# Performance work log

Measured on AMD Instinct MI355X. Metric: run time of the kernel, lower is better.

The kernel has to match this reference:

```python
import jax, jax.numpy as jnp
import numpy as np

B, C, H, W = 8, 512, 32, 32
NUM_HEADS = 8
NUM_GROUPS = 32
EPS = 1e-5


def setup_inputs() -> dict:
    key = jax.random.key(0)
    k1, k2, k3 = jax.random.split(key, 3)
    x = jax.random.normal(k1, (B, C, H, W), dtype=jnp.float32)
    gn_w = jnp.ones((C,), dtype=jnp.float32)
    gn_b = jnp.zeros((C,), dtype=jnp.float32)
    qkv_w = jax.random.normal(k2, (3 * C, C), dtype=jnp.float32) * 0.02
    qkv_b = jnp.zeros((3 * C,), dtype=jnp.float32)
    # NOTE: original zero-initializes proj_out; we use random weights so the
    # residual branch is non-trivial for correctness testing.
    proj_w = jax.random.normal(k3, (C, C), dtype=jnp.float32) * 0.02
    proj_b = jnp.zeros((C,), dtype=jnp.float32)
    return {"x": x, "gn_w": gn_w, "gn_b": gn_b, "qkv_w": qkv_w,
            "qkv_b": qkv_b, "proj_w": proj_w, "proj_b": proj_b}


def _group_norm(x, w, b):
    # x: [B, C, T]
    Bn, Cn, T = x.shape
    xg = x.reshape(Bn, NUM_GROUPS, Cn // NUM_GROUPS, T)
    mean = xg.mean(axis=(2, 3), keepdims=True)
    var = xg.var(axis=(2, 3), keepdims=True)
    xn = ((xg - mean) * jax.lax.rsqrt(var + EPS)).reshape(Bn, Cn, T)
    return xn * w[None, :, None] + b[None, :, None]


def reference(x, gn_w, gn_b, qkv_w, qkv_b, proj_w, proj_b):
    b, c = x.shape[0], x.shape[1]
    spatial = x.shape[2:]
    xr = x.reshape(b, c, -1)                      # [B, C, T]
    xn = _group_norm(xr, gn_w, gn_b)
    # 1x1 conv1d: [3C, C] x [B, C, T] -> [B, 3C, T]
    qkv = jnp.einsum('oc,bct->bot', qkv_w, xn) + qkv_b[None, :, None]
    T = qkv.shape[-1]
    qkv = qkv.reshape(b * NUM_HEADS, -1, T)       # [B*Nh, 3*ch, T]
    ch = qkv.shape[1] // 3
    q, k, v = jnp.split(qkv, 3, axis=1)
    scale = 1.0 / np.sqrt(np.sqrt(ch))
    weight = jnp.einsum('bct,bcs->bts', q * scale, k * scale)  # [B*Nh, T, T]
    weight = jax.nn.softmax(weight.astype(jnp.float32), axis=-1).astype(weight.dtype)
    h = jnp.einsum('bts,bcs->bct', weight, v)     # [B*Nh, ch, T]
    h = h.reshape(b, c, T)
    h = jnp.einsum('oc,bct->bot', proj_w, h) + proj_b[None, :, None]
    return (xr + h).reshape(b, c, *spatial)
```

## Files before the change

### kernel.cpp

```cpp
#include <hip/hip_runtime.h>
#include <math.h>

#define Bn 8
#define Cn 512
#define Tn 1024

typedef __attribute__((ext_vector_type(8))) short bf16x8;
typedef __attribute__((ext_vector_type(4))) float f32x4;

__device__ __forceinline__ unsigned short f2bf(float f) {
  unsigned int u = __builtin_bit_cast(unsigned int, f);
  u = (u + 0x7FFFu + ((u >> 16) & 1u)) >> 16;
  return (unsigned short)u;
}

__device__ __forceinline__ unsigned int cvtpk_bf16(float lo, float hi) {
  unsigned int r;
  asm("v_cvt_pk_bf16_f32 %0, %1, %2" : "=v"(r) : "v"(lo), "v"(hi));
  return r;
}

typedef __attribute__((address_space(1))) const unsigned int GU32;
typedef __attribute__((address_space(3))) unsigned int LU32;
__device__ __forceinline__ void gld16(const unsigned short* g, unsigned short* l) {
  __builtin_amdgcn_global_load_lds((GU32*)g, (LU32*)l, 16, 0, 0);
}

__device__ __forceinline__ void stage128x64(const unsigned short* __restrict__ src,
                                            size_t row_stride, unsigned short* lds, int tid) {
  const int w = tid >> 6;
  const int row = tid >> 3;
  const int sc = (tid & 7) ^ ((tid >> 3) & 7);
#pragma unroll
  for (int c = 0; c < 4; ++c)
    gld16(src + (size_t)(c * 32 + row) * row_stride + sc * 8,
          (unsigned short*)((char*)lds + c * 4096 + w * 1024));
}

__device__ __forceinline__ void stage64x64(const unsigned short* __restrict__ src,
                                           size_t row_stride, unsigned short* lds, int tid) {
  const int w = tid >> 6;
  const int row = tid >> 3;
  const int sc = (tid & 7) ^ ((tid >> 3) & 7);
#pragma unroll
  for (int c = 0; c < 2; ++c)
    gld16(src + (size_t)(c * 32 + row) * row_stride + sc * 8,
          (unsigned short*)((char*)lds + c * 4096 + w * 1024));
}

__global__ __launch_bounds__(256) void gn_kernel(const float* __restrict__ x,
                                                 const float* __restrict__ gw,
                                                 const float* __restrict__ gb,
                                                 unsigned short* __restrict__ xn_t) {
  const int blk = blockIdx.x;
  const int b = blk >> 5, g = blk & 31;
  const size_t base = ((size_t)b * Cn + (size_t)g * 16) * Tn;
  const float4* __restrict__ xin = (const float4*)(x + base);
  const int tid = threadIdx.x;

  float vv[16][4];
  float sum = 0.f, sq = 0.f;
#pragma unroll
  for (int k = 0; k < 16; ++k) {
    const float4 t4 = xin[tid + (k << 8)];
    vv[k][0] = t4.x; vv[k][1] = t4.y; vv[k][2] = t4.z; vv[k][3] = t4.w;
    sum += t4.x + t4.y + t4.z + t4.w;
    sq += t4.x * t4.x + t4.y * t4.y + t4.z * t4.z + t4.w * t4.w;
  }

  __shared__ float rs[8];
  const int lane = tid & 63, wv = tid >> 6;
#pragma unroll
  for (int off = 32; off > 0; off >>= 1) {
    sum += __shfl_down(sum, off);
    sq += __shfl_down(sq, off);
  }
  if (lane == 0) { rs[wv] = sum; rs[4 + wv] = sq; }
  __syncthreads();
  const float ts = rs[0] + rs[1] + rs[2] + rs[3];
  const float tq = rs[4] + rs[5] + rs[6] + rs[7];
  const float mean = ts * (1.f / 16384.f);
  const float var = tq * (1.f / 16384.f) - mean * mean;
  const float rstd = rsqrtf(var + 1e-5f);

  float aa[16], bb[16];
#pragma unroll
  for (int k = 0; k < 16; ++k) {
    aa[k] = rstd * gw[g * 16 + k];
    bb[k] = gb[g * 16 + k] - mean * aa[k];
  }

#pragma unroll
  for (int j = 0; j < 4; ++j) {
    const int t = tid * 4 + j;
    unsigned int pk[8];
#pragma unroll
    for (int k2 = 0; k2 < 8; ++k2) {
      const unsigned int lo = f2bf(vv[2 * k2][j] * aa[2 * k2] + bb[2 * k2]);
      const unsigned int hi = f2bf(vv[2 * k2 + 1][j] * aa[2 * k2 + 1] + bb[2 * k2 + 1]);
      pk[k2] = lo | (hi << 16);
    }
    unsigned short* dst = xn_t + ((size_t)(b * Tn + t)) * Cn + g * 16;
    *(uint4*)dst = make_uint4(pk[0], pk[1], pk[2], pk[3]);
    *((uint4*)dst + 1) = make_uint4(pk[4], pk[5], pk[6], pk[7]);
  }
}

__global__ __launch_bounds__(256) void cvt_kernel(const float* __restrict__ src,
                                                  unsigned short* __restrict__ dst, int n4) {
  const int i = blockIdx.x * 256 + threadIdx.x;
  if (i < n4) {
    const float4 f = ((const float4*)src)[i];
    uint2 o;
    o.x = (unsigned int)f2bf(f.x) | ((unsigned int)f2bf(f.y) << 16);
    o.y = (unsigned int)f2bf(f.z) | ((unsigned int)f2bf(f.w) << 16);
    ((uint2*)dst)[i] = o;
  }
}

__global__ __launch_bounds__(256, 2) void qkv_gemm(const unsigned short* __restrict__ Wb,
                                                   const unsigned short* __restrict__ Xb,
                                                   const float* __restrict__ bias,
                                                   unsigned short* __restrict__ q_t,
                                                   unsigned short* __restrict__ k_t,
                                                   unsigned short* __restrict__ v_t) {
  __shared__ unsigned short As[2][8192];
  __shared__ unsigned short Bs[2][8192];
  const int id = blockIdx.x;
  const int b = id & 7;
  const int inner = id >> 3;
  const int bx = inner % 12, by = inner / 12;
  const int o0 = bx * 128, t0 = by * 128;
  const int tid = threadIdx.x, lane = tid & 63, w = tid >> 6;
  const int wr = w >> 1, wc = w & 1;
  const int ln = lane & 15, g16 = lane >> 4;
  const unsigned short* __restrict__ X = Xb + (size_t)b * Tn * Cn;
  const unsigned short* __restrict__ Wt = Wb + (size_t)o0 * 512;
  const unsigned short* __restrict__ Xt = X + (size_t)t0 * 512;

  f32x4 acc[4][4];
#pragma unroll
  for (int mt = 0; mt < 4; ++mt)
#pragma unroll
    for (int nt = 0; nt < 4; ++nt) acc[mt][nt] = (f32x4){0.f, 0.f, 0.f, 0.f};

  stage128x64(Wt, 512, &As[0][0], tid);
  stage128x64(Xt, 512, &Bs[0][0], tid);
  __syncthreads();

  int buf = 0;
  for (int k0 = 0; k0 < 512; k0 += 64) {
    if (k0 + 64 < 512) {
      stage128x64(Wt + k0 + 64, 512, &As[buf ^ 1][0], tid);
      stage128x64(Xt + k0 + 64, 512, &Bs[buf ^ 1][0], tid);
    }
    const char* Ab = (const char*)&As[buf][0];
    const char* Bb = (const char*)&Bs[buf][0];
    bf16x8 af[4][2], bfr[4][2];
#pragma unroll
    for (int mt = 0; mt < 4; ++mt)
#pragma unroll
      for (int kk = 0; kk < 2; ++kk) {
        const int row = wr * 64 + mt * 16 + ln;
        const int c16 = ((kk << 2) | g16) ^ (ln & 7);
        af[mt][kk] = *(const bf16x8*)(Ab + row * 128 + (c16 << 4));
      }
#pragma unroll
    for (int nt = 0; nt < 4; ++nt)
#pragma unroll
      for (int kk = 0; kk < 2; ++kk) {
        const int row = wc * 64 + nt * 16 + ln;
        const int c16 = ((kk << 2) | g16) ^ (ln & 7);
        bfr[nt][kk] = *(const bf16x8*)(Bb + row * 128 + (c16 << 4));
      }
#pragma unroll
    for (int kk = 0; kk < 2; ++kk)
#pragma unroll
      for (int mt = 0; mt < 4; ++mt)
#pragma unroll
        for (int nt = 0; nt < 4; ++nt)
          acc[mt][nt] =
              __builtin_amdgcn_mfma_f32_16x16x32_bf16(af[mt][kk], bfr[nt][kk], acc[mt][nt], 0, 0, 0);
    __syncthreads();
    buf ^= 1;
  }

  const int o_base = o0 + wr * 64, t_base = t0 + wc * 64;
  const int partw = (o_base >> 6) % 3;
  const int bh = b * 8 + o_base / 192;
  unsigned short (*Vlds)[136] = (unsigned short (*)[136])(&As[0][0]);

  if (partw < 2) {
    unsigned short* qk = (partw == 0 ? q_t : k_t) + (size_t)bh * 65536;
    const float sc = (partw == 0) ? 0.18033688f : 1.0f;
#pragma unroll
    for (int mt = 0; mt < 4; ++mt) {
      const int ob16 = o_base + mt * 16;
      float bv[4];
#pragma unroll
      for (int r = 0; r < 4; ++r) bv[r] = bias[ob16 + g16 * 4 + r];
#pragma unroll
      for (int nt = 0; nt < 4; ++nt) {
        const int t = t_base + nt * 16 + ln;
        const float v0 = (acc[mt][nt][0] + bv[0]) * sc;
        const float v1 = (acc[mt][nt][1] + bv[1]) * sc;
        const float v2 = (acc[mt][nt][2] + bv[2]) * sc;
        const float v3 = (acc[mt][nt][3] + bv[3]) * sc;
        uint2 pk;
        pk.x = (unsigned int)f2bf(v0) | ((unsigned int)f2bf(v1) << 16);
        pk.y = (unsigned int)f2bf(v2) | ((unsigned int)f2bf(v3) << 16);
        *(uint2*)(qk + (size_t)t * 64 + mt * 16 + g16 * 4) = pk;
      }
    }
  } else {
#pragma unroll
    for (int mt = 0; mt < 4; ++mt) {
      float bv[4];
#pragma unroll
      for (int r = 0; r < 4; ++r) bv[r] = bias[o_base + mt * 16 + g16 * 4 + r];
#pragma unroll
      for (int nt = 0; nt < 4; ++nt)
#pragma unroll
        for (int r = 0; r < 4; ++r)
          Vlds[mt * 16 + g16 * 4 + r][wc * 64 + nt * 16 + ln] = f2bf(acc[mt][nt][r] + bv[r]);
    }
  }
  __syncthreads();
  const int bxm = bx % 3;
  if (bxm) {
    const int o_first = o0 + (bxm - 1) * 64;
    unsigned short* vdst = v_t + (size_t)(b * 8 + o_first / 192) * 65536;
    const int c = tid >> 2, tseg = (tid & 3) << 5;
    const unsigned short* src = &Vlds[c][tseg];
    unsigned short* p = vdst + (size_t)c * Tn + t0 + tseg;
    const uint4 d0 = *(const uint4*)(src);
    const uint4 d1 = *(const uint4*)(src + 8);
    const uint4 d2 = *(const uint4*)(src + 16);
    const uint4 d3 = *(const uint4*)(src + 24);
    *(uint4*)(p) = d0;
    *(uint4*)(p + 8) = d1;
    *(uint4*)(p + 16) = d2;
    *(uint4*)(p + 24) = d3;
  }
}

__global__ __launch_bounds__(256, 3) void attn_kernel(const unsigned short* __restrict__ q_t,
                                                      const unsigned short* __restrict__ k_t,
                                                      const unsigned short* __restrict__ v_t,
                                                      unsigned short* __restrict__ h_t) {
  __shared__ unsigned short Ks[2][4096];
  __shared__ unsigned short Vs[2][4096];
  __shared__ __align__(16) unsigned short P_lds[4][1024];
  const int id = blockIdx.x;
  const int xcd = id & 7, qq = id >> 3;
  const int bh = ((qq >> 4) << 3) | xcd;
  const int tc = qq & 15;
  const int tid = threadIdx.x, lane = tid & 63, w = tid >> 6;
  const int t_wave = tc * 64 + w * 16;
  const int ln = lane & 15, g16 = lane >> 4, g8 = g16 * 8;
  const unsigned short* __restrict__ qbase = q_t + (size_t)bh * 65536;
  const unsigned short* __restrict__ kbase = k_t + (size_t)bh * 65536;
  const unsigned short* __restrict__ vbase = v_t + (size_t)bh * 65536;
  char* __restrict__ Pb = (char*)P_lds[w];

  int koff[4][2];
#pragma unroll
  for (int f = 0; f < 4; ++f)
#pragma unroll
    for (int kb = 0; kb < 2; ++kb)
      koff[f][kb] = (f * 16 + ln) * 128 + ((((kb << 2) | g16) ^ (ln & 7)) << 4);

  int wr_off[4], rd_off[2];
#pragma unroll
  for (int ns = 0; ns < 4; ++ns)
    wr_off[ns] = ln * 128 + ((((ns << 1) | (g16 >> 1)) ^ (ln & 7)) << 4) + ((g16 & 1) << 3);
#pragma unroll
  for (int kb = 0; kb < 2; ++kb)
    rd_off[kb] = ln * 128 + ((((kb << 2) | g16) ^ (ln & 7)) << 4);

  bf16x8 qf[2];
#pragma unroll
  for (int kb = 0; kb < 2; ++kb)
    qf[kb] = *(const bf16x8*)(qbase + (size_t)(t_wave + ln) * 64 + kb * 32 + g8);

  f32x4 o_acc[4];
#pragma unroll
  for (int nc = 0; nc < 4; ++nc) o_acc[nc] = (f32x4){0.f, 0.f, 0.f, 0.f};
  float m_run = -1e30f, l_run = 0.f;

  stage64x64(kbase, 64, &Ks[0][0], tid);
  stage64x64(vbase, 1024, &Vs[0][0], tid);
  __syncthreads();

  int buf = 0;
  for (int st = 0; st < 16; ++st) {
    const int s0 = st << 6;
    if (st < 15) {
      stage64x64(kbase + (size_t)(s0 + 64) * 64, 64, &Ks[buf ^ 1][0], tid);
      stage64x64(vbase + (s0 + 64), 1024, &Vs[buf ^ 1][0], tid);
    }
    const char* Kb = (const char*)&Ks[buf][0];
    const char* Vb = (const char*)&Vs[buf][0];

    bf16x8 kf[4][2];
#pragma unroll
    for (int ns = 0; ns < 4; ++ns)
#pragma unroll
      for (int kb = 0; kb < 2; ++kb)
        kf[ns][kb] = *(const bf16x8*)(Kb + koff[ns][kb]);

    f32x4 sacc[4];
#pragma unroll
    for (int ns = 0; ns < 4; ++ns) sacc[ns] = (f32x4){0.f, 0.f, 0.f, 0.f};

    __builtin_amdgcn_s_setprio(1);
#pragma unroll
    for (int kb = 0; kb < 2; ++kb)
#pragma unroll
      for (int ns = 0; ns < 4; ++ns)
        sacc[ns] = __builtin_amdgcn_mfma_f32_16x16x32_bf16(kf[ns][kb], qf[kb], sacc[ns], 0, 0, 0);
    __builtin_amdgcn_s_setprio(0);

    bf16x8 vf[4][2];
#pragma unroll
    for (int nc = 0; nc < 4; ++nc)
#pragma unroll
      for (int kb = 0; kb < 2; ++kb)
        vf[nc][kb] = *(const bf16x8*)(Vb + koff[nc][kb]);

    float m = sacc[0][0];
#pragma unroll
    for (int ns = 0; ns < 4; ++ns)
#pragma unroll
      for (int r = 0; r < 4; ++r) m = fmaxf(m, sacc[ns][r]);
    m = fmaxf(m, __shfl_xor(m, 16));
    m = fmaxf(m, __shfl_xor(m, 32));

    if (__any((m > m_run + 11.f) ? 1 : 0)) {
      const float mnew = fmaxf(m_run, m);
      const float al = __builtin_amdgcn_exp2f(m_run - mnew);
      m_run = mnew;
      l_run *= al;
      float al4[4];
#pragma unroll
      for (int r = 0; r < 4; ++r) al4[r] = __shfl(al, (g16 << 2) + r);
#pragma unroll
      for (int nc = 0; nc < 4; ++nc)
#pragma unroll
        for (int r = 0; r < 4; ++r) o_acc[nc][r] *= al4[r];
    }

    float rsum = 0.f;
#pragma unroll
    for (int ns = 0; ns < 4; ++ns) {
#pragma unroll
      for (int r = 0; r < 4; ++r) {
        sacc[ns][r] = __builtin_amdgcn_exp2f(sacc[ns][r] - m_run);
        rsum += sacc[ns][r];
      }
    }
    rsum += __shfl_xor(rsum, 16);
    rsum += __shfl_xor(rsum, 32);
    l_run += rsum;

#pragma unroll
    for (int ns = 0; ns < 4; ++ns) {
      uint2 pk2;
      pk2.x = cvtpk_bf16(sacc[ns][0], sacc[ns][1]);
      pk2.y = cvtpk_bf16(sacc[ns][2], sacc[ns][3]);
      *(uint2*)(Pb + wr_off[ns]) = pk2;
    }
    bf16x8 pf[2];
#pragma unroll
    for (int kb = 0; kb < 2; ++kb) pf[kb] = *(const bf16x8*)(Pb + rd_off[kb]);

    __builtin_amdgcn_s_setprio(1);
#pragma unroll
    for (int kb = 0; kb < 2; ++kb)
#pragma unroll
      for (int nc = 0; nc < 4; ++nc)
        o_acc[nc] = __builtin_amdgcn_mfma_f32_16x16x32_bf16(pf[kb], vf[nc][kb], o_acc[nc], 0, 0, 0);
    __builtin_amdgcn_s_setprio(0);

    __syncthreads();
    buf ^= 1;
  }

  const float rl = 1.f / l_run;
  float rl4[4];
#pragma unroll
  for (int r = 0; r < 4; ++r) rl4[r] = __shfl(rl, (g16 << 2) + r);
  const int b = bh >> 3, hh = bh & 7;
  unsigned short* __restrict__ hb = h_t + (size_t)b * Tn * Cn + hh * 64;
#pragma unroll
  for (int nc = 0; nc < 4; ++nc) {
    const int c = nc * 16 + ln;
#pragma unroll
    for (int r = 0; r < 4; ++r) {
      const int t = t_wave + g16 * 4 + r;
      hb[(size_t)t * Cn + c] = f2bf(o_acc[nc][r] * rl4[r]);
    }
  }
}

__global__ __launch_bounds__(256, 2) void proj_gemm(const unsigned short* __restrict__ Wb,
                                                    const unsigned short* __restrict__ Hb,
                                                    const float* __restrict__ pbias,
                                                    const float* __restrict__ x,
                                                    float* __restrict__ out) {
  __shared__ unsigned short As[2][8192];
  __shared__ unsigned short Bs[2][8192];
  const int id = blockIdx.x;
  const int b = id & 7;
  const int inner = id >> 3;
  const int bx = inner & 3, by = inner >> 2;
  const int o0 = bx * 128, t0 = by * 128;
  const int tid = threadIdx.x, lane = tid & 63, w = tid >> 6;
  const int wr = w >> 1, wc = w & 1;
  const int ln = lane & 15, g16 = lane >> 4;
  const unsigned short* __restrict__ H = Hb + (size_t)b * Tn * Cn;
  const unsigned short* __restrict__ Wt = Wb + (size_t)o0 * 512;
  const unsigned short* __restrict__ Ht = H + (size_t)t0 * 512;

  f32x4 acc[4][4];
#pragma unroll
  for (int mt = 0; mt < 4; ++mt)
#pragma unroll
    for (int nt = 0; nt < 4; ++nt) acc[mt][nt] = (f32x4){0.f, 0.f, 0.f, 0.f};

  stage128x64(Wt, 512, &As[0][0], tid);
  stage128x64(Ht, 512, &Bs[0][0], tid);
  __syncthreads();

  int buf = 0;
  for (int k0 = 0; k0 < 512; k0 += 64) {
    if (k0 + 64 < 512) {
      stage128x64(Wt + k0 + 64, 512, &As[buf ^ 1][0], tid);
      stage128x64(Ht + k0 + 64, 512, &Bs[buf ^ 1][0], tid);
    }
    const char* Ab = (const char*)&As[buf][0];
    const char* Bb = (const char*)&Bs[buf][0];
    bf16x8 af[4][2], bfr[4][2];
#pragma unroll
    for (int mt = 0; mt < 4; ++mt)
#pragma unroll
      for (int kk = 0; kk < 2; ++kk) {
        const int row = wr * 64 + mt * 16 + ln;
        const int c16 = ((kk << 2) | g16) ^ (ln & 7);
        af[mt][kk] = *(const bf16x8*)(Ab + row * 128 + (c16 << 4));
      }
#pragma unroll
    for (int nt = 0; nt < 4; ++nt)
#pragma unroll
      for (int kk = 0; kk < 2; ++kk) {
        const int row = wc * 64 + nt * 16 + ln;
        const int c16 = ((kk << 2) | g16) ^ (ln & 7);
        bfr[nt][kk] = *(const bf16x8*)(Bb + row * 128 + (c16 << 4));
      }
#pragma unroll
    for (int kk = 0; kk < 2; ++kk)
#pragma unroll
      for (int mt = 0; mt < 4; ++mt)
#pragma unroll
        for (int nt = 0; nt < 4; ++nt)
          acc[mt][nt] =
              __builtin_amdgcn_mfma_f32_16x16x32_bf16(af[mt][kk], bfr[nt][kk], acc[mt][nt], 0, 0, 0);
    __syncthreads();
    buf ^= 1;
  }

  const int o_base = o0 + wr * 64, t_base = t0 + wc * 64;
#pragma unroll
  for (int mt = 0; mt < 4; ++mt) {
    const int ob = o_base + mt * 16 + g16 * 4;
    float pb[4];
#pragma unroll
    for (int r = 0; r < 4; ++r) pb[r] = pbias[ob + r];
#pragma unroll
    for (int nt = 0; nt < 4; ++nt) {
      const int t = t_base + nt * 16 + ln;
#pragma unroll
      for (int r = 0; r < 4; ++r) {
        const size_t idx = (size_t)b * Cn * Tn + (size_t)(ob + r) * Tn + t;
        out[idx] = acc[mt][nt][r] + pb[r] + x[idx];
      }
    }
  }
}

extern "C" void kernel_launch(void* const* d_in, const int* in_sizes, int n_in,
                              void* d_out, int out_size, void* d_ws, size_t ws_size,
                              hipStream_t stream) {
  (void)in_sizes; (void)n_in; (void)out_size; (void)ws_size;
  const float* x = (const float*)d_in[0];
  const float* gn_w = (const float*)d_in[1];
  const float* gn_b = (const float*)d_in[2];
  const float* qkv_w = (const float*)d_in[3];
  const float* qkv_b = (const float*)d_in[4];
  const float* proj_w = (const float*)d_in[5];
  const float* proj_b = (const float*)d_in[6];
  float* out = (float*)d_out;

  unsigned short* wsu = (unsigned short*)d_ws;
  unsigned short* xn_t = wsu;
  unsigned short* wqkv = xn_t + (size_t)4194304;
  unsigned short* wproj = wqkv + (size_t)786432;
  unsigned short* q_t = wproj + (size_t)262144;
  unsigned short* k_t = q_t + (size_t)4194304;
  unsigned short* v_t = k_t + (size_t)4194304;
  unsigned short* h_t = v_t + (size_t)4194304;

  gn_kernel<<<dim3(256), 256, 0, stream>>>(x, gn_w, gn_b, xn_t);
  cvt_kernel<<<dim3(768), 256, 0, stream>>>(qkv_w, wqkv, 196608);
  cvt_kernel<<<dim3(256), 256, 0, stream>>>(proj_w, wproj, 65536);
  qkv_gemm<<<dim3(768), 256, 0, stream>>>(wqkv, xn_t, qkv_b, q_t, k_t, v_t);
  attn_kernel<<<dim3(1024), 256, 0, stream>>>(q_t, k_t, v_t, h_t);
  proj_gemm<<<dim3(256), 256, 0, stream>>>(wproj, h_t, proj_b, x, out);
}
```

Before: 158.0 us.

## Process two query tiles per wave in attention and merge weight conversions

Each attention wave now handles 32 query rows (two 16-row M tiles) instead of 16. Every K/V fragment read from LDS therefore feeds twice as many MFMAs, and the block count is halved. This raises register use: launch bounds drop from 3 to 2 blocks per CU, and the P staging buffer doubles. The two fp32-to-bf16 weight conversion launches are also merged into one kernel to save a launch.

```diff
diff --git a/kernel.cpp b/kernel.cpp
--- a/kernel.cpp
+++ b/kernel.cpp
@@ -106,16 +106,19 @@
   }
 }
 
-__global__ __launch_bounds__(256) void cvt_kernel(const float* __restrict__ src,
-                                                  unsigned short* __restrict__ dst, int n4) {
-  const int i = blockIdx.x * 256 + threadIdx.x;
-  if (i < n4) {
-    const float4 f = ((const float4*)src)[i];
-    uint2 o;
-    o.x = (unsigned int)f2bf(f.x) | ((unsigned int)f2bf(f.y) << 16);
-    o.y = (unsigned int)f2bf(f.z) | ((unsigned int)f2bf(f.w) << 16);
-    ((uint2*)dst)[i] = o;
-  }
+__global__ __launch_bounds__(256) void cvt2_kernel(const float* __restrict__ qkv_w,
+                                                   const float* __restrict__ proj_w,
+                                                   unsigned short* __restrict__ wqkv,
+                                                   unsigned short* __restrict__ wproj) {
+  const int blk = blockIdx.x;
+  const float* src = (blk < 768) ? qkv_w : proj_w;
+  unsigned short* dst = (blk < 768) ? wqkv : wproj;
+  const int i = ((blk < 768) ? blk : blk - 768) * 256 + threadIdx.x;
+  const float4 f = ((const float4*)src)[i];
+  uint2 o;
+  o.x = (unsigned int)f2bf(f.x) | ((unsigned int)f2bf(f.y) << 16);
+  o.y = (unsigned int)f2bf(f.z) | ((unsigned int)f2bf(f.w) << 16);
+  ((uint2*)dst)[i] = o;
 }
 
 __global__ __launch_bounds__(256, 2) void qkv_gemm(const unsigned short* __restrict__ Wb,
@@ -244,19 +247,19 @@
   }
 }
 
-__global__ __launch_bounds__(256, 3) void attn_kernel(const unsigned short* __restrict__ q_t,
+__global__ __launch_bounds__(256, 2) void attn_kernel(const unsigned short* __restrict__ q_t,
                                                       const unsigned short* __restrict__ k_t,
                                                       const unsigned short* __restrict__ v_t,
                                                       unsigned short* __restrict__ h_t) {
   __shared__ unsigned short Ks[2][4096];
   __shared__ unsigned short Vs[2][4096];
-  __shared__ __align__(16) unsigned short P_lds[4][1024];
+  __shared__ __align__(16) unsigned short P_lds[4][2048];
   const int id = blockIdx.x;
   const int xcd = id & 7, qq = id >> 3;
-  const int bh = ((qq >> 4) << 3) | xcd;
-  const int tc = qq & 15;
+  const int b = qq >> 3, tc = qq & 7;
+  const int bh = b * 8 + xcd;
   const int tid = threadIdx.x, lane = tid & 63, w = tid >> 6;
-  const int t_wave = tc * 64 + w * 16;
+  const int t_wave = tc * 128 + w * 32;
   const int ln = lane & 15, g16 = lane >> 4, g8 = g16 * 8;
   const unsigned short* __restrict__ qbase = q_t + (size_t)bh * 65536;
   const unsigned short* __restrict__ kbase = k_t + (size_t)bh * 65536;
@@ -278,15 +281,19 @@
   for (int kb = 0; kb < 2; ++kb)
     rd_off[kb] = ln * 128 + ((((kb << 2) | g16) ^ (ln & 7)) << 4);
 
-  bf16x8 qf[2];
-#pragma unroll
-  for (int kb = 0; kb < 2; ++kb)
-    qf[kb] = *(const bf16x8*)(qbase + (size_t)(t_wave + ln) * 64 + kb * 32 + g8);
-
-  f32x4 o_acc[4];
-#pragma unroll
-  for (int nc = 0; nc < 4; ++nc) o_acc[nc] = (f32x4){0.f, 0.f, 0.f, 0.f};
-  float m_run = -1e30f, l_run = 0.f;
+  bf16x8 qf[2][2];
+#pragma unroll
+  for (int mt = 0; mt < 2; ++mt)
+#pragma unroll
+    for (int kb = 0; kb < 2; ++kb)
+      qf[mt][kb] = *(const bf16x8*)(qbase + (size_t)(t_wave + mt * 16 + ln) * 64 + kb * 32 + g8);
+
+  f32x4 o_acc[2][4];
+#pragma unroll
+  for (int mt = 0; mt < 2; ++mt)
+#pragma unroll
+    for (int nc = 0; nc < 4; ++nc) o_acc[mt][nc] = (f32x4){0.f, 0.f, 0.f, 0.f};
+  float m_run[2] = {-1e30f, -1e30f}, l_run[2] = {0.f, 0.f};
 
   stage64x64(kbase, 64, &Ks[0][0], tid);
   stage64x64(vbase, 1024, &Vs[0][0], tid);
@@ -309,17 +316,82 @@
       for (int kb = 0; kb < 2; ++kb)
         kf[ns][kb] = *(const bf16x8*)(Kb + koff[ns][kb]);
 
-    f32x4 sacc[4];
-#pragma unroll
-    for (int ns = 0; ns < 4; ++ns) sacc[ns] = (f32x4){0.f, 0.f, 0.f, 0.f};
+    f32x4 sacc[2][4];
+#pragma unroll
+    for (int mt = 0; mt < 2; ++mt)
+#pragma unroll
+      for (int ns = 0; ns < 4; ++ns) sacc[mt][ns] = (f32x4){0.f, 0.f, 0.f, 0.f};
 
     __builtin_amdgcn_s_setprio(1);
 #pragma unroll
     for (int kb = 0; kb < 2; ++kb)
 #pragma unroll
+      for (int ns = 0; ns < 4; ++ns) {
+        sacc[0][ns] = __builtin_amdgcn_mfma_f32_16x16x32_bf16(kf[ns][kb], qf[0][kb], sacc[0][ns], 0, 0, 0);
+        sacc[1][ns] = __builtin_amdgcn_mfma_f32_16x16x32_bf16(kf[ns][kb], qf[1][kb], sacc[1][ns], 0, 0, 0);
+      }
+    __builtin_amdgcn_s_setprio(0);
+
+    float m[2];
+#pragma unroll
+    for (int mt = 0; mt < 2; ++mt) {
+      float mm = sacc[mt][0][0];
+#pragma unroll
       for (int ns = 0; ns < 4; ++ns)
-        sacc[ns] = __builtin_amdgcn_mfma_f32_16x16x32_bf16(kf[ns][kb], qf[kb], sacc[ns], 0, 0, 0);
-    __builtin_amdgcn_s_setprio(0);
+#pragma unroll
+        for (int r = 0; r < 4; ++r) mm = fmaxf(mm, sacc[mt][ns][r]);
+      mm = fmaxf(mm, __shfl_xor(mm, 16));
+      mm = fmaxf(mm, __shfl_xor(mm, 32));
+      m[mt] = mm;
+    }
+
+    const bool need = (m[0] > m_run[0] + 11.f) || (m[1] > m_run[1] + 11.f);
+    if (__any(need ? 1 : 0)) {
+#pragma unroll
+      for (int mt = 0; mt < 2; ++mt) {
+        const float mnew = fmaxf(m_run[mt], m[mt]);
+        const float al = __builtin_amdgcn_exp2f(m_run[mt] - mnew);
+        m_run[mt] = mnew;
+        l_run[mt] *= al;
+        float al4[4];
+#pragma unroll
+        for (int r = 0; r < 4; ++r) al4[r] = __shfl(al, (g16 << 2) + r);
+#pragma unroll
+        for (int nc = 0; nc < 4; ++nc)
+#pragma unroll
+          for (int r = 0; r < 4; ++r) o_acc[mt][nc][r] *= al4[r];
+      }
+    }
+
+#pragma unroll
+    for (int mt = 0; mt < 2; ++mt) {
+      float rsum = 0.f;
+#pragma unroll
+      for (int ns = 0; ns < 4; ++ns) {
+#pragma unroll
+        for (int r = 0; r < 4; ++r) {
+          sacc[mt][ns][r] = __builtin_amdgcn_exp2f(sacc[mt][ns][r] - m_run[mt]);
+          rsum += sacc[mt][ns][r];
+        }
+      }
+      rsum += __shfl_xor(rsum, 16);
+      rsum += __shfl_xor(rsum, 32);
+      l_run[mt] += rsum;
+#pragma unroll
+      for (int ns = 0; ns < 4; ++ns) {
+        uint2 pk2;
+        pk2.x = cvtpk_bf16(sacc[mt][ns][0], sacc[mt][ns][1]);
+        pk2.y = cvtpk_bf16(sacc[mt][ns][2], sacc[mt][ns][3]);
+        *(uint2*)(Pb + mt * 2048 + wr_off[ns]) = pk2;
+      }
+    }
+
+    bf16x8 pf[2][2];
+#pragma unroll
+    for (int mt = 0; mt < 2; ++mt)
+#pragma unroll
+      for (int kb = 0; kb < 2; ++kb)
+        pf[mt][kb] = *(const bf16x8*)(Pb + mt * 2048 + rd_off[kb]);
 
     bf16x8 vf[4][2];
 #pragma unroll
@@ -328,77 +400,36 @@
       for (int kb = 0; kb < 2; ++kb)
         vf[nc][kb] = *(const bf16x8*)(Vb + koff[nc][kb]);
 
-    float m = sacc[0][0];
-#pragma unroll
-    for (int ns = 0; ns < 4; ++ns)
-#pragma unroll
-      for (int r = 0; r < 4; ++r) m = fmaxf(m, sacc[ns][r]);
-    m = fmaxf(m, __shfl_xor(m, 16));
-    m = fmaxf(m, __shfl_xor(m, 32));
-
-    if (__any((m > m_run + 11.f) ? 1 : 0)) {
-      const float mnew = fmaxf(m_run, m);
-      const float al = __builtin_amdgcn_exp2f(m_run - mnew);
-      m_run = mnew;
-      l_run *= al;
-      float al4[4];
-#pragma unroll
-      for (int r = 0; r < 4; ++r) al4[r] = __shfl(al, (g16 << 2) + r);
-#pragma unroll
-      for (int nc = 0; nc < 4; ++nc)
-#pragma unroll
-        for (int r = 0; r < 4; ++r) o_acc[nc][r] *= al4[r];
-    }
-
-    float rsum = 0.f;
-#pragma unroll
-    for (int ns = 0; ns < 4; ++ns) {
-#pragma unroll
-      for (int r = 0; r < 4; ++r) {
-        sacc[ns][r] = __builtin_amdgcn_exp2f(sacc[ns][r] - m_run);
-        rsum += sacc[ns][r];
-      }
-    }
-    rsum += __shfl_xor(rsum, 16);
-    rsum += __shfl_xor(rsum, 32);
-    l_run += rsum;
-
-#pragma unroll
-    for (int ns = 0; ns < 4; ++ns) {
-      uint2 pk2;
-      pk2.x = cvtpk_bf16(sacc[ns][0], sacc[ns][1]);
-      pk2.y = cvtpk_bf16(sacc[ns][2], sacc[ns][3]);
-      *(uint2*)(Pb + wr_off[ns]) = pk2;
-    }
-    bf16x8 pf[2];
-#pragma unroll
-    for (int kb = 0; kb < 2; ++kb) pf[kb] = *(const bf16x8*)(Pb + rd_off[kb]);
-
     __builtin_amdgcn_s_setprio(1);
 #pragma unroll
     for (int kb = 0; kb < 2; ++kb)
 #pragma unroll
-      for (int nc = 0; nc < 4; ++nc)
-        o_acc[nc] = __builtin_amdgcn_mfma_f32_16x16x32_bf16(pf[kb], vf[nc][kb], o_acc[nc], 0, 0, 0);
+      for (int nc = 0; nc < 4; ++nc) {
+        o_acc[0][nc] = __builtin_amdgcn_mfma_f32_16x16x32_bf16(pf[0][kb], vf[nc][kb], o_acc[0][nc], 0, 0, 0);
+        o_acc[1][nc] = __builtin_amdgcn_mfma_f32_16x16x32_bf16(pf[1][kb], vf[nc][kb], o_acc[1][nc], 0, 0, 0);
+      }
     __builtin_amdgcn_s_setprio(0);
 
     __syncthreads();
     buf ^= 1;
   }
 
-  const float rl = 1.f / l_run;
-  float rl4[4];
-#pragma unroll
-  for (int r = 0; r < 4; ++r) rl4[r] = __shfl(rl, (g16 << 2) + r);
-  const int b = bh >> 3, hh = bh & 7;
-  unsigned short* __restrict__ hb = h_t + (size_t)b * Tn * Cn + hh * 64;
-#pragma unroll
-  for (int nc = 0; nc < 4; ++nc) {
-    const int c = nc * 16 + ln;
-#pragma unroll
-    for (int r = 0; r < 4; ++r) {
-      const int t = t_wave + g16 * 4 + r;
-      hb[(size_t)t * Cn + c] = f2bf(o_acc[nc][r] * rl4[r]);
+  const int bb = bh >> 3, hh = bh & 7;
+  unsigned short* __restrict__ hb = h_t + (size_t)bb * Tn * Cn + hh * 64;
+#pragma unroll
+  for (int mt = 0; mt < 2; ++mt) {
+    const float rl = 1.f / l_run[mt];
+    float rl4[4];
+#pragma unroll
+    for (int r = 0; r < 4; ++r) rl4[r] = __shfl(rl, (g16 << 2) + r);
+#pragma unroll
+    for (int nc = 0; nc < 4; ++nc) {
+      const int c = nc * 16 + ln;
+#pragma unroll
+      for (int r = 0; r < 4; ++r) {
+        const int t = t_wave + mt * 16 + g16 * 4 + r;
+        hb[(size_t)t * Cn + c] = f2bf(o_acc[mt][nc][r] * rl4[r]);
+      }
     }
   }
 }
@@ -511,9 +542,8 @@
   unsigned short* h_t = v_t + (size_t)4194304;
 
   gn_kernel<<<dim3(256), 256, 0, stream>>>(x, gn_w, gn_b, xn_t);
-  cvt_kernel<<<dim3(768), 256, 0, stream>>>(qkv_w, wqkv, 196608);
-  cvt_kernel<<<dim3(256), 256, 0, stream>>>(proj_w, wproj, 65536);
+  cvt2_kernel<<<dim3(1024), 256, 0, stream>>>(qkv_w, proj_w, wqkv, wproj);
   qkv_gemm<<<dim3(768), 256, 0, stream>>>(wqkv, xn_t, qkv_b, q_t, k_t, v_t);
-  attn_kernel<<<dim3(1024), 256, 0, stream>>>(q_t, k_t, v_t, h_t);
+  attn_kernel<<<dim3(512), 256, 0, stream>>>(q_t, k_t, v_t, h_t);
   proj_gemm<<<dim3(256), 256, 0, stream>>>(wproj, h_t, proj_b, x, out);
 }
```

Result: faster. 154.8 us (-2.0%).
